# Kernel optimization log

Measured on AMD Instinct MI355X. Metric: run time of the kernel, lower is better.

Reference implementation:

```python
import jax, jax.numpy as jnp
import numpy as np

N_NODES = 100000
N_EDGES = 1600000
F_IN = 256
DIM = 128
N_CLASSES = 16


def gcn_conv(x, W, b, src, dst, num_nodes):
    # PyG GCNConv: add self-loops, symmetric normalization D^-1/2 (A+I) D^-1/2,
    # linear transform then scatter-add aggregation at destination nodes.
    loops = jnp.arange(num_nodes)
    s = jnp.concatenate([src, loops])
    d = jnp.concatenate([dst, loops])
    deg = jax.ops.segment_sum(jnp.ones(d.shape[0], dtype=x.dtype), d, num_segments=num_nodes)
    dinv = jnp.where(deg > 0, jax.lax.rsqrt(deg), jnp.zeros_like(deg))
    norm = dinv[s] * dinv[d]                       # [E+N]
    h = x @ W                                      # [N, out] transform-then-propagate
    msg = h[s] * norm[:, None]                     # gather + scale
    out = jax.ops.segment_sum(msg, d, num_segments=num_nodes)  # scatter-add
    return out + b


def setup_inputs() -> dict:
    key = jax.random.key(0)
    k1, k2, k3, k4 = jax.random.split(key, 4)
    x = jax.random.normal(k1, (N_NODES, F_IN), dtype=jnp.float32)
    edge_index = jax.random.randint(k2, (2, N_EDGES), 0, N_NODES, dtype=jnp.int64)
    W1 = jax.random.normal(k3, (F_IN, DIM), dtype=jnp.float32) * 0.05
    b1 = jnp.zeros((DIM,), dtype=jnp.float32)
    W2 = jax.random.normal(k4, (DIM, N_CLASSES), dtype=jnp.float32) * 0.05
    b2 = jnp.zeros((N_CLASSES,), dtype=jnp.float32)
    return {"x": x, "edge_index": edge_index, "W1": W1, "b1": b1, "W2": W2, "b2": b2}


def reference(x, edge_index, W1, b1, W2, b2):
    # Gcn.forward with num_layers=2 (gcs empty), eval-mode dropout (identity)
    src, dst = edge_index[0], edge_index[1]
    n = x.shape[0]
    h = jax.nn.relu(gcn_conv(x, W1, b1, src, dst, n))
    logits = gcn_conv(h, W2, b2, src, dst, n)
    return jax.nn.log_softmax(logits, axis=-1)
```

## Files before the change

kernel.cpp:

```cpp
#include <hip/hip_runtime.h>
#include <hip/hip_bf16.h>

#define F_IN   256
#define DIM    128
#define NCLS   16
#define BSH    9
#define NBMAX  256
#define CAP    10240
#define PCAP   14336

typedef short bf16x8 __attribute__((ext_vector_type(8)));
typedef float f32x4  __attribute__((ext_vector_type(4)));
typedef float f32x2  __attribute__((ext_vector_type(2)));

__device__ __forceinline__ unsigned short f2bf(float f) {
    union { float f; unsigned u; } v; v.f = f;
    unsigned r = v.u + 0x7fffu + ((v.u >> 16) & 1u);
    return (unsigned short)(r >> 16);
}
__device__ __forceinline__ float bflo(unsigned v) { return __uint_as_float(v << 16); }
__device__ __forceinline__ float bfhi(unsigned v) { return __uint_as_float(v & 0xffff0000u); }


__global__ void binit_kernel(int* __restrict__ bucketCur) {
    int t = threadIdx.x;
    if (t < NBMAX) bucketCur[t] = t * CAP;
}

__global__ __launch_bounds__(1024) void part_kernel(const int* __restrict__ src,
                                                    const int* __restrict__ dst,
                                                    int* __restrict__ bucketCur,
                                                    int2* __restrict__ pairs, int E) {
    __shared__ int hist[NBMAX];
    __shared__ int pos[NBMAX];
    int t = threadIdx.x;
    int base = blockIdx.x * 8192;
    int s[8], d[8];
#pragma unroll
    for (int k = 0; k < 8; k++) {
        int i = base + k * 1024 + t;
        bool v = (i < E);
        s[k] = v ? src[i] : 0;
        d[k] = v ? dst[i] : -1;
    }
    if (t < NBMAX) hist[t] = 0;
    __syncthreads();
#pragma unroll
    for (int k = 0; k < 8; k++)
        if (d[k] >= 0) atomicAdd(&hist[d[k] >> BSH], 1);
    __syncthreads();
    if (t < NBMAX && hist[t]) pos[t] = atomicAdd(&bucketCur[t], hist[t]);
    __syncthreads();
#pragma unroll
    for (int k = 0; k < 8; k++)
        if (d[k] >= 0) {
            int p = atomicAdd(&pos[d[k] >> BSH], 1);
            pairs[p] = make_int2(s[k], d[k]);
        }
}

__global__ __launch_bounds__(256) void csr_kernel(const int2* __restrict__ pairs,
                                                  const int* __restrict__ bucketCur,
                                                  int* __restrict__ rowInfo, float* __restrict__ dinv,
                                                  int* __restrict__ col, int N) {
    __shared__ int cnt[512];
    __shared__ int part[256];
    int b = blockIdx.x, t = threadIdx.x;
    int n0 = b << BSH;
    int nn = N - n0; if (nn > 512) nn = 512;
    int in0 = b * CAP;
    int inEnd = bucketCur[b];
    int out0 = b * PCAP;

    if (t < 256) { cnt[t] = 0; cnt[t + 256] = 0; }
    __syncthreads();
    for (int p = in0 + t; p < inEnd; p += 256)
        atomicAdd(&cnt[pairs[p].y - n0], 1);
    __syncthreads();

    int i0 = t * 2;
    int c0 = cnt[i0], c1 = cnt[i0 + 1];
    int p0 = (c0 + 7) & ~7, p1 = (c1 + 7) & ~7;
    int tsum = p0 + p1;
    part[t] = tsum;
    __syncthreads();
    for (int off = 1; off < 256; off <<= 1) {
        int u = (t >= off) ? part[t - off] : 0;
        __syncthreads();
        part[t] += u;
        __syncthreads();
    }
    int run = out0 + part[t] - tsum;
    int e0 = run, e1 = e0 + p0;
    __syncthreads();
    if (i0 + 0 < nn) { rowInfo[n0 + i0 + 0] = ((e0 >> 3) << 12) | (p0 >> 3); dinv[n0 + i0 + 0] = rsqrtf((float)(c0 + 1)); }
    if (i0 + 1 < nn) { rowInfo[n0 + i0 + 1] = ((e1 >> 3) << 12) | (p1 >> 3); dinv[n0 + i0 + 1] = rsqrtf((float)(c1 + 1)); }
    cnt[i0] = e0; cnt[i0 + 1] = e1;
    __syncthreads();

    for (int p = in0 + t; p < inEnd; p += 256) {
        int2 e = pairs[p];
        int q = atomicAdd(&cnt[e.y - n0], 1);
        col[q] = e.x;
    }
    __syncthreads();
    if (i0 + 0 < nn) for (int q = c0; q < p0; q++) col[e0 + q] = N;
    if (i0 + 1 < nn) for (int q = c1; q < p1; q++) col[e1 + q] = N;
}

__global__ void w1prep_kernel(const float* __restrict__ W1, unsigned short* __restrict__ W1f,
                              unsigned* __restrict__ h1dummy, unsigned* __restrict__ h2dummy) {
    int t = blockIdx.x * blockDim.x + threadIdx.x;
    if (blockIdx.x == 0) {
        if (threadIdx.x < 32) h1dummy[threadIdx.x] = 0;
        else if (threadIdx.x < 40) h2dummy[threadIdx.x - 32] = 0;
    }
    if (t >= 8 * 32 * 16 * 8) return;
    int j = t & 7, c = (t >> 3) & 15, g = (t >> 7) & 31, f = t >> 12;
    W1f[t] = f2bf(W1[(g * 8 + j) * DIM + f * 16 + c]);
}

__global__ __launch_bounds__(256) void gemm1_mfma(const float* __restrict__ X,
                                                  const unsigned short* __restrict__ W1f,
                                                  const float* __restrict__ dinv,
                                                  unsigned char* __restrict__ H1, int M) {
    int tid = threadIdx.x;
    int wm = tid >> 6, l = tid & 63;
    int lr = l & 15, lg = l >> 4;
    int bm = blockIdx.x * 64 + wm * 16;

    f32x4 acc[8];
#pragma unroll
    for (int f = 0; f < 8; f++) acc[f] = (f32x4){0.f, 0.f, 0.f, 0.f};

#pragma unroll
    for (int s = 0; s < 8; s++) {
        int r = bm + lr;
        r = (r < M) ? r : (M - 1);
        const float* xp = X + (size_t)r * F_IN + s * 32 + lg * 8;
        float4 u0 = *(const float4*)xp;
        float4 u1 = *(const float4*)(xp + 4);
        bf16x8 a;
        a[0] = (short)f2bf(u0.x); a[1] = (short)f2bf(u0.y);
        a[2] = (short)f2bf(u0.z); a[3] = (short)f2bf(u0.w);
        a[4] = (short)f2bf(u1.x); a[5] = (short)f2bf(u1.y);
        a[6] = (short)f2bf(u1.z); a[7] = (short)f2bf(u1.w);
#pragma unroll
        for (int f = 0; f < 8; f++) {
            const unsigned short* bp = W1f + ((((f * 32 + s * 4 + lg) * 16) + lr) << 3);
            bf16x8 b = *(const bf16x8*)bp;
            acc[f] = __builtin_amdgcn_mfma_f32_16x16x32_bf16(a, b, acc[f], 0, 0, 0);
        }
    }
#pragma unroll
    for (int r = 0; r < 4; r++) {
        int row = bm + lg * 4 + r;
        if (row < M) {
            float di = dinv[row];
            float v0 = di * acc[0][r], v1 = di * acc[1][r];
            float v2 = di * acc[2][r], v3 = di * acc[3][r];
            float v4 = di * acc[4][r], v5 = di * acc[5][r];
            float v6 = di * acc[6][r], v7 = di * acc[7][r];
            int w0 = __builtin_amdgcn_cvt_pk_fp8_f32(v0, v1, 0, false);
            w0 = __builtin_amdgcn_cvt_pk_fp8_f32(v2, v3, w0, true);
            int w1 = __builtin_amdgcn_cvt_pk_fp8_f32(v4, v5, 0, false);
            w1 = __builtin_amdgcn_cvt_pk_fp8_f32(v6, v7, w1, true);
            uint2 pk; pk.x = (unsigned)w0; pk.y = (unsigned)w1;
            *(uint2*)(H1 + ((size_t)row << 7) + lr * 8) = pk;
        }
    }
}

__global__ __launch_bounds__(256, 8) void agg1_kernel(const unsigned char* __restrict__ H1,
                                                      const int* __restrict__ rowInfo,
                                                      const int* __restrict__ col,
                                                      const float* __restrict__ dinv,
                                                      const float* __restrict__ b1,
                                                      const float* __restrict__ W2,
                                                      unsigned short* __restrict__ H2, int N) {
    __shared__ f32x4 a_lds4[4][32];
    int tid = threadIdx.x;
    int wave = tid >> 6, lane = tid & 63;
    int d = blockIdx.x * 4 + wave;
    int half = lane >> 5;
    int li = lane & 31;
    unsigned kb4 = (unsigned)li * 4;

    float di = 0.f;
    if (d < N) {
        di = dinv[d];
        unsigned sg = *(const unsigned*)(H1 + (((unsigned)d << 7) | kb4));
        if (half) sg = 0u;
        f32x2 acc01 = __builtin_amdgcn_cvt_pk_f32_fp8((int)sg, false);
        f32x2 acc23 = __builtin_amdgcn_cvt_pk_f32_fp8((int)sg, true);

        int info = rowInfo[d];
        int jb = (info >> 12) << 3;
        int jend = jb + ((info & 0xFFF) << 3);
        for (int j0 = jb; j0 < jend; j0 += 64) {
            int cnt = jend - j0; if (cnt > 64) cnt = 64;
            int eidx = col[j0 + lane];
            for (int kk = 0; kk < cnt; kk += 8) {
                int sA = __shfl(eidx, kk + 0 + half);
                int sB = __shfl(eidx, kk + 2 + half);
                int sC = __shfl(eidx, kk + 4 + half);
                int sD = __shfl(eidx, kk + 6 + half);
                unsigned gA = *(const unsigned*)(H1 + (((unsigned)sA << 7) | kb4));
                unsigned gB = *(const unsigned*)(H1 + (((unsigned)sB << 7) | kb4));
                unsigned gC = *(const unsigned*)(H1 + (((unsigned)sC << 7) | kb4));
                unsigned gD = *(const unsigned*)(H1 + (((unsigned)sD << 7) | kb4));
                f32x2 a0 = __builtin_amdgcn_cvt_pk_f32_fp8((int)gA, false);
                f32x2 a1 = __builtin_amdgcn_cvt_pk_f32_fp8((int)gA, true);
                f32x2 b0 = __builtin_amdgcn_cvt_pk_f32_fp8((int)gB, false);
                f32x2 b1v = __builtin_amdgcn_cvt_pk_f32_fp8((int)gB, true);
                f32x2 c0 = __builtin_amdgcn_cvt_pk_f32_fp8((int)gC, false);
                f32x2 c1 = __builtin_amdgcn_cvt_pk_f32_fp8((int)gC, true);
                f32x2 d0 = __builtin_amdgcn_cvt_pk_f32_fp8((int)gD, false);
                f32x2 d1 = __builtin_amdgcn_cvt_pk_f32_fp8((int)gD, true);
                acc01 += (a0 + b0) + (c0 + d0);
                acc23 += (a1 + b1v) + (c1 + d1);
            }
        }
        acc01.x += __shfl_xor(acc01.x, 32);
        acc01.y += __shfl_xor(acc01.y, 32);
        acc23.x += __shfl_xor(acc23.x, 32);
        acc23.y += __shfl_xor(acc23.y, 32);
        if (half == 0) {
            int p0 = li * 4;
            int f0 = ((p0 & 7) << 4) | (p0 >> 3);
            int f1 = (((p0 + 1) & 7) << 4) | ((p0 + 1) >> 3);
            int f2 = (((p0 + 2) & 7) << 4) | ((p0 + 2) >> 3);
            int f3 = (((p0 + 3) & 7) << 4) | ((p0 + 3) >> 3);
            f32x4 a;
            a[0] = fmaxf(fmaf(acc01.x, di, b1[f0]), 0.f);
            a[1] = fmaxf(fmaf(acc01.y, di, b1[f1]), 0.f);
            a[2] = fmaxf(fmaf(acc23.x, di, b1[f2]), 0.f);
            a[3] = fmaxf(fmaf(acc23.y, di, b1[f3]), 0.f);
            a_lds4[wave][li] = a;
        }
    }
    __syncthreads();
    if (d < N) {
        int c = lane & 15, kg = lane >> 4;
        const float* a_ldsf = (const float*)a_lds4[wave];
        const float* w2b = W2 + kg * 64 + c;
        float p = 0.f;
#pragma unroll
        for (int i = 0; i < 32; i++) {
            int w2off = ((i & 7) << 8) + ((i >> 3) << 4);
            p = fmaf(a_ldsf[kg * 32 + i], w2b[w2off], p);
        }
        p += __shfl_xor(p, 16);
        p += __shfl_xor(p, 32);
        if (lane < 16) H2[(size_t)d * NCLS + c] = f2bf(p * di);
    }
}

__global__ __launch_bounds__(256, 8) void agg2_kernel(const unsigned short* __restrict__ H2,
                                                      const int* __restrict__ rowInfo,
                                                      const int* __restrict__ col,
                                                      const float* __restrict__ dinv,
                                                      const float* __restrict__ b2,
                                                      float* __restrict__ OUT, int N) {
    int tid = threadIdx.x;
    int g = tid >> 3, q = tid & 7;
    int d = blockIdx.x * 32 + g;
    if (d >= N) return;
    unsigned cb = (unsigned)q * 4;
    const char* H2b = (const char*)H2;
    float di = dinv[d];
    unsigned u = *(const unsigned*)(H2b + (((unsigned)d << 5) | cb));
    f32x2 acc; acc.x = bflo(u); acc.y = bfhi(u);
    int info = rowInfo[d];
    int jb = (info >> 12) << 3;
    int jend = jb + ((info & 0xFFF) << 3);
    for (int j = jb; j < jend; j += 8) {
        unsigned u0 = *(const unsigned*)(H2b + (((unsigned)col[j + 0] << 5) | cb));
        unsigned u1 = *(const unsigned*)(H2b + (((unsigned)col[j + 1] << 5) | cb));
        unsigned u2 = *(const unsigned*)(H2b + (((unsigned)col[j + 2] << 5) | cb));
        unsigned u3 = *(const unsigned*)(H2b + (((unsigned)col[j + 3] << 5) | cb));
        unsigned u4 = *(const unsigned*)(H2b + (((unsigned)col[j + 4] << 5) | cb));
        unsigned u5 = *(const unsigned*)(H2b + (((unsigned)col[j + 5] << 5) | cb));
        unsigned u6 = *(const unsigned*)(H2b + (((unsigned)col[j + 6] << 5) | cb));
        unsigned u7 = *(const unsigned*)(H2b + (((unsigned)col[j + 7] << 5) | cb));
        f32x2 v0; v0.x = bflo(u0); v0.y = bfhi(u0);
        f32x2 v1; v1.x = bflo(u1); v1.y = bfhi(u1);
        f32x2 v2; v2.x = bflo(u2); v2.y = bfhi(u2);
        f32x2 v3; v3.x = bflo(u3); v3.y = bfhi(u3);
        f32x2 v4; v4.x = bflo(u4); v4.y = bfhi(u4);
        f32x2 v5; v5.x = bflo(u5); v5.y = bfhi(u5);
        f32x2 v6; v6.x = bflo(u6); v6.y = bfhi(u6);
        f32x2 v7; v7.x = bflo(u7); v7.y = bfhi(u7);
        acc += ((v0 + v1) + (v2 + v3)) + ((v4 + v5) + (v6 + v7));
    }
    float l0 = fmaf(acc.x, di, b2[q * 2]);
    float l1 = fmaf(acc.y, di, b2[q * 2 + 1]);
    float m = fmaxf(l0, l1);
    m = fmaxf(m, __shfl_xor(m, 1, 8));
    m = fmaxf(m, __shfl_xor(m, 2, 8));
    m = fmaxf(m, __shfl_xor(m, 4, 8));
    float e = __expf(l0 - m) + __expf(l1 - m);
    e += __shfl_xor(e, 1, 8);
    e += __shfl_xor(e, 2, 8);
    e += __shfl_xor(e, 4, 8);
    float ls = __logf(e);
    float2 o; o.x = l0 - m - ls; o.y = l1 - m - ls;
    *(float2*)(OUT + ((size_t)d << 4) + q * 2) = o;
}

extern "C" void kernel_launch(void* const* d_in, const int* in_sizes, int n_in,
                              void* d_out, int out_size, void* d_ws, size_t ws_size,
                              hipStream_t stream) {
    const float* x  = (const float*)d_in[0];
    const int*   ei = (const int*)d_in[1];
    const float* W1 = (const float*)d_in[2];
    const float* b1 = (const float*)d_in[3];
    const float* W2 = (const float*)d_in[4];
    const float* b2 = (const float*)d_in[5];
    float* out = (float*)d_out;

    const int N = in_sizes[0] / F_IN;
    const int E = in_sizes[1] / 2;
    const int* src = ei;
    const int* dst = ei + E;
    const int nb = (N + (1 << BSH) - 1) >> BSH;

    char* ws = (char*)d_ws;
    size_t off = 0;
    auto alloc = [&](size_t bytes) {
        size_t o = off;
        off += (bytes + 255) & ~(size_t)255;
        return (void*)(ws + o);
    };
    int*            bucketCur   = (int*)alloc(NBMAX * 4);
    int*            rowInfo     = (int*)alloc((size_t)N * 4);
    float*          dinv        = (float*)alloc((size_t)N * 4);
    int*            colw        = (int*)alloc((size_t)NBMAX * PCAP * 4);
    unsigned short* w1f         = (unsigned short*)alloc(32768 * 2);
    unsigned short* h2          = (unsigned short*)alloc((size_t)(N + 1) * NCLS * 2);
    size_t uni = (size_t)NBMAX * CAP * 8;
    size_t h1b = (size_t)(N + 1) * DIM;
    if (h1b > uni) uni = h1b;
    char*           ureg        = (char*)alloc(uni);
    int2*           pairs       = (int2*)ureg;
    unsigned char*  h1          = (unsigned char*)ureg;
    (void)ws_size;

    const int gridE = (E + 8191) / 8192;

    binit_kernel<<<1, NBMAX, 0, stream>>>(bucketCur);
    part_kernel<<<gridE, 1024, 0, stream>>>(src, dst, bucketCur, pairs, E);
    csr_kernel<<<nb, 256, 0, stream>>>(pairs, bucketCur, rowInfo, dinv, colw, N);

    w1prep_kernel<<<128, 256, 0, stream>>>(W1, w1f,
                                           (unsigned*)(h1 + (size_t)N * DIM),
                                           (unsigned*)(h2 + (size_t)N * NCLS));
    gemm1_mfma<<<(N + 63) / 64, 256, 0, stream>>>(x, w1f, dinv, h1, N);
    agg1_kernel<<<(N + 3) / 4, 256, 0, stream>>>(h1, rowInfo, colw, dinv, b1, W2, h2, N);
    agg2_kernel<<<(N + 31) / 32, 256, 0, stream>>>(h2, rowInfo, colw, dinv, b2, out, N);
}
```

Measured before the change: 154.1 us.

## Overlap CSR build with GEMM1 by moving source-side dinv scaling into aggregation

Merges W1 prep with bucket init into one kernel, and fuses CSR construction and the X·W1 MFMA GEMM into a single launch whose blocks split by index. The GEMM no longer needs dinv, so it can run alongside the CSR build. To allow this, the source-side degree normalisation moves into agg1, which gathers dinv per neighbour and uses FMAs. pairs and H1 now get separate buffers instead of sharing one, and row padding grows to multiples of 16 so agg1 can unroll 16 gathers. The costs are more padding entries, extra dinv gathers and shuffles, and fp8 quantisation of unscaled values, which could change accuracy.

New measurement: 143.6 us. 6.8% less time.

```diff
diff --git a/kernel.cpp b/kernel.cpp
--- a/kernel.cpp
+++ b/kernel.cpp
@@ -7,7 +7,7 @@
 #define BSH    9
 #define NBMAX  256
 #define CAP    10240
-#define PCAP   14336
+#define PCAP   18432
 
 typedef short bf16x8 __attribute__((ext_vector_type(8)));
 typedef float f32x4  __attribute__((ext_vector_type(4)));
@@ -21,10 +21,20 @@
 __device__ __forceinline__ float bflo(unsigned v) { return __uint_as_float(v << 16); }
 __device__ __forceinline__ float bfhi(unsigned v) { return __uint_as_float(v & 0xffff0000u); }
 
-
-__global__ void binit_kernel(int* __restrict__ bucketCur) {
-    int t = threadIdx.x;
-    if (t < NBMAX) bucketCur[t] = t * CAP;
+__global__ void init_kernel(const float* __restrict__ W1, unsigned short* __restrict__ W1f,
+                            int* __restrict__ bucketCur,
+                            unsigned* __restrict__ h1dummy, unsigned* __restrict__ h2dummy,
+                            float* __restrict__ dinv, int N) {
+    int t = blockIdx.x * blockDim.x + threadIdx.x;
+    if (blockIdx.x == 0) {
+        bucketCur[threadIdx.x] = threadIdx.x * CAP;
+        if (threadIdx.x < 32) h1dummy[threadIdx.x] = 0;
+        else if (threadIdx.x < 40) h2dummy[threadIdx.x - 32] = 0;
+        else if (threadIdx.x == 40) dinv[N] = 0.f;
+    }
+    if (t >= 8 * 32 * 16 * 8) return;
+    int j = t & 7, c = (t >> 3) & 15, g = (t >> 7) & 31, f = t >> 12;
+    W1f[t] = f2bf(W1[(g * 8 + j) * DIM + f * 16 + c]);
 }
 
 __global__ __launch_bounds__(1024) void part_kernel(const int* __restrict__ src,
@@ -59,114 +69,97 @@
         }
 }
 
-__global__ __launch_bounds__(256) void csr_kernel(const int2* __restrict__ pairs,
-                                                  const int* __restrict__ bucketCur,
-                                                  int* __restrict__ rowInfo, float* __restrict__ dinv,
-                                                  int* __restrict__ col, int N) {
+__global__ __launch_bounds__(256) void csr_gemm_kernel(
+        const int2* __restrict__ pairs, const int* __restrict__ bucketCur,
+        int* __restrict__ rowInfo, float* __restrict__ dinv, int* __restrict__ col,
+        const float* __restrict__ X, const unsigned short* __restrict__ W1f,
+        unsigned char* __restrict__ H1, int N, int nbCsr) {
     __shared__ int cnt[512];
     __shared__ int part[256];
-    int b = blockIdx.x, t = threadIdx.x;
-    int n0 = b << BSH;
-    int nn = N - n0; if (nn > 512) nn = 512;
-    int in0 = b * CAP;
-    int inEnd = bucketCur[b];
-    int out0 = b * PCAP;
-
-    if (t < 256) { cnt[t] = 0; cnt[t + 256] = 0; }
-    __syncthreads();
-    for (int p = in0 + t; p < inEnd; p += 256)
-        atomicAdd(&cnt[pairs[p].y - n0], 1);
-    __syncthreads();
-
-    int i0 = t * 2;
-    int c0 = cnt[i0], c1 = cnt[i0 + 1];
-    int p0 = (c0 + 7) & ~7, p1 = (c1 + 7) & ~7;
-    int tsum = p0 + p1;
-    part[t] = tsum;
-    __syncthreads();
-    for (int off = 1; off < 256; off <<= 1) {
-        int u = (t >= off) ? part[t - off] : 0;
-        __syncthreads();
-        part[t] += u;
-        __syncthreads();
-    }
-    int run = out0 + part[t] - tsum;
-    int e0 = run, e1 = e0 + p0;
-    __syncthreads();
-    if (i0 + 0 < nn) { rowInfo[n0 + i0 + 0] = ((e0 >> 3) << 12) | (p0 >> 3); dinv[n0 + i0 + 0] = rsqrtf((float)(c0 + 1)); }
-    if (i0 + 1 < nn) { rowInfo[n0 + i0 + 1] = ((e1 >> 3) << 12) | (p1 >> 3); dinv[n0 + i0 + 1] = rsqrtf((float)(c1 + 1)); }
-    cnt[i0] = e0; cnt[i0 + 1] = e1;
-    __syncthreads();
-
-    for (int p = in0 + t; p < inEnd; p += 256) {
-        int2 e = pairs[p];
-        int q = atomicAdd(&cnt[e.y - n0], 1);
-        col[q] = e.x;
-    }
-    __syncthreads();
-    if (i0 + 0 < nn) for (int q = c0; q < p0; q++) col[e0 + q] = N;
-    if (i0 + 1 < nn) for (int q = c1; q < p1; q++) col[e1 + q] = N;
-}
-
-__global__ void w1prep_kernel(const float* __restrict__ W1, unsigned short* __restrict__ W1f,
-                              unsigned* __restrict__ h1dummy, unsigned* __restrict__ h2dummy) {
-    int t = blockIdx.x * blockDim.x + threadIdx.x;
-    if (blockIdx.x == 0) {
-        if (threadIdx.x < 32) h1dummy[threadIdx.x] = 0;
-        else if (threadIdx.x < 40) h2dummy[threadIdx.x - 32] = 0;
-    }
-    if (t >= 8 * 32 * 16 * 8) return;
-    int j = t & 7, c = (t >> 3) & 15, g = (t >> 7) & 31, f = t >> 12;
-    W1f[t] = f2bf(W1[(g * 8 + j) * DIM + f * 16 + c]);
-}
-
-__global__ __launch_bounds__(256) void gemm1_mfma(const float* __restrict__ X,
-                                                  const unsigned short* __restrict__ W1f,
-                                                  const float* __restrict__ dinv,
-                                                  unsigned char* __restrict__ H1, int M) {
-    int tid = threadIdx.x;
-    int wm = tid >> 6, l = tid & 63;
-    int lr = l & 15, lg = l >> 4;
-    int bm = blockIdx.x * 64 + wm * 16;
-
-    f32x4 acc[8];
-#pragma unroll
-    for (int f = 0; f < 8; f++) acc[f] = (f32x4){0.f, 0.f, 0.f, 0.f};
-
-#pragma unroll
-    for (int s = 0; s < 8; s++) {
-        int r = bm + lr;
-        r = (r < M) ? r : (M - 1);
-        const float* xp = X + (size_t)r * F_IN + s * 32 + lg * 8;
-        float4 u0 = *(const float4*)xp;
-        float4 u1 = *(const float4*)(xp + 4);
-        bf16x8 a;
-        a[0] = (short)f2bf(u0.x); a[1] = (short)f2bf(u0.y);
-        a[2] = (short)f2bf(u0.z); a[3] = (short)f2bf(u0.w);
-        a[4] = (short)f2bf(u1.x); a[5] = (short)f2bf(u1.y);
-        a[6] = (short)f2bf(u1.z); a[7] = (short)f2bf(u1.w);
-#pragma unroll
-        for (int f = 0; f < 8; f++) {
-            const unsigned short* bp = W1f + ((((f * 32 + s * 4 + lg) * 16) + lr) << 3);
-            bf16x8 b = *(const bf16x8*)bp;
-            acc[f] = __builtin_amdgcn_mfma_f32_16x16x32_bf16(a, b, acc[f], 0, 0, 0);
-        }
-    }
-#pragma unroll
-    for (int r = 0; r < 4; r++) {
-        int row = bm + lg * 4 + r;
-        if (row < M) {
-            float di = dinv[row];
-            float v0 = di * acc[0][r], v1 = di * acc[1][r];
-            float v2 = di * acc[2][r], v3 = di * acc[3][r];
-            float v4 = di * acc[4][r], v5 = di * acc[5][r];
-            float v6 = di * acc[6][r], v7 = di * acc[7][r];
-            int w0 = __builtin_amdgcn_cvt_pk_fp8_f32(v0, v1, 0, false);
-            w0 = __builtin_amdgcn_cvt_pk_fp8_f32(v2, v3, w0, true);
-            int w1 = __builtin_amdgcn_cvt_pk_fp8_f32(v4, v5, 0, false);
-            w1 = __builtin_amdgcn_cvt_pk_fp8_f32(v6, v7, w1, true);
-            uint2 pk; pk.x = (unsigned)w0; pk.y = (unsigned)w1;
-            *(uint2*)(H1 + ((size_t)row << 7) + lr * 8) = pk;
+    int t = threadIdx.x;
+
+    if (blockIdx.x < nbCsr) {
+        int b = blockIdx.x;
+        int n0 = b << BSH;
+        int nn = N - n0; if (nn > 512) nn = 512;
+        int in0 = b * CAP;
+        int inEnd = bucketCur[b];
+        int out0 = b * PCAP;
+
+        cnt[t] = 0; cnt[t + 256] = 0;
+        __syncthreads();
+        for (int p = in0 + t; p < inEnd; p += 256)
+            atomicAdd(&cnt[pairs[p].y - n0], 1);
+        __syncthreads();
+
+        int i0 = t * 2;
+        int c0 = cnt[i0], c1 = cnt[i0 + 1];
+        int p0 = (c0 + 15) & ~15, p1 = (c1 + 15) & ~15;
+        int tsum = p0 + p1;
+        part[t] = tsum;
+        __syncthreads();
+        for (int off = 1; off < 256; off <<= 1) {
+            int u = (t >= off) ? part[t - off] : 0;
+            __syncthreads();
+            part[t] += u;
+            __syncthreads();
+        }
+        int run = out0 + part[t] - tsum;
+        int e0 = run, e1 = e0 + p0;
+        __syncthreads();
+        if (i0 + 0 < nn) { rowInfo[n0 + i0 + 0] = ((e0 >> 4) << 12) | (p0 >> 4); dinv[n0 + i0 + 0] = rsqrtf((float)(c0 + 1)); }
+        if (i0 + 1 < nn) { rowInfo[n0 + i0 + 1] = ((e1 >> 4) << 12) | (p1 >> 4); dinv[n0 + i0 + 1] = rsqrtf((float)(c1 + 1)); }
+        cnt[i0] = e0; cnt[i0 + 1] = e1;
+        __syncthreads();
+
+        for (int p = in0 + t; p < inEnd; p += 256) {
+            int2 e = pairs[p];
+            int q = atomicAdd(&cnt[e.y - n0], 1);
+            col[q] = e.x;
+        }
+        __syncthreads();
+        if (i0 + 0 < nn) for (int q = c0; q < p0; q++) col[e0 + q] = N;
+        if (i0 + 1 < nn) for (int q = c1; q < p1; q++) col[e1 + q] = N;
+    } else {
+        int gb = blockIdx.x - nbCsr;
+        int wm = t >> 6, l = t & 63;
+        int lr = l & 15, lg = l >> 4;
+        int bm = gb * 64 + wm * 16;
+
+        f32x4 acc[8];
+#pragma unroll
+        for (int f = 0; f < 8; f++) acc[f] = (f32x4){0.f, 0.f, 0.f, 0.f};
+
+#pragma unroll
+        for (int s = 0; s < 8; s++) {
+            int r = bm + lr;
+            r = (r < N) ? r : (N - 1);
+            const float* xp = X + (size_t)r * F_IN + s * 32 + lg * 8;
+            float4 u0 = *(const float4*)xp;
+            float4 u1 = *(const float4*)(xp + 4);
+            bf16x8 a;
+            a[0] = (short)f2bf(u0.x); a[1] = (short)f2bf(u0.y);
+            a[2] = (short)f2bf(u0.z); a[3] = (short)f2bf(u0.w);
+            a[4] = (short)f2bf(u1.x); a[5] = (short)f2bf(u1.y);
+            a[6] = (short)f2bf(u1.z); a[7] = (short)f2bf(u1.w);
+#pragma unroll
+            for (int f = 0; f < 8; f++) {
+                const unsigned short* bp = W1f + ((((f * 32 + s * 4 + lg) * 16) + lr) << 3);
+                bf16x8 b = *(const bf16x8*)bp;
+                acc[f] = __builtin_amdgcn_mfma_f32_16x16x32_bf16(a, b, acc[f], 0, 0, 0);
+            }
+        }
+#pragma unroll
+        for (int r = 0; r < 4; r++) {
+            int row = bm + lg * 4 + r;
+            if (row < N) {
+                int w0 = __builtin_amdgcn_cvt_pk_fp8_f32(acc[0][r], acc[1][r], 0, false);
+                w0 = __builtin_amdgcn_cvt_pk_fp8_f32(acc[2][r], acc[3][r], w0, true);
+                int w1 = __builtin_amdgcn_cvt_pk_fp8_f32(acc[4][r], acc[5][r], 0, false);
+                w1 = __builtin_amdgcn_cvt_pk_fp8_f32(acc[6][r], acc[7][r], w1, true);
+                uint2 pk; pk.x = (unsigned)w0; pk.y = (unsigned)w1;
+                *(uint2*)(H1 + ((size_t)row << 7) + lr * 8) = pk;
+            }
         }
     }
 }
@@ -191,34 +184,70 @@
         di = dinv[d];
         unsigned sg = *(const unsigned*)(H1 + (((unsigned)d << 7) | kb4));
         if (half) sg = 0u;
-        f32x2 acc01 = __builtin_amdgcn_cvt_pk_f32_fp8((int)sg, false);
-        f32x2 acc23 = __builtin_amdgcn_cvt_pk_f32_fp8((int)sg, true);
+        f32x2 s0v = __builtin_amdgcn_cvt_pk_f32_fp8((int)sg, false);
+        f32x2 s1v = __builtin_amdgcn_cvt_pk_f32_fp8((int)sg, true);
+        f32x2 acc01, acc23;
+        acc01.x = s0v.x * di; acc01.y = s0v.y * di;
+        acc23.x = s1v.x * di; acc23.y = s1v.y * di;
 
         int info = rowInfo[d];
-        int jb = (info >> 12) << 3;
-        int jend = jb + ((info & 0xFFF) << 3);
+        int jb = (info >> 12) << 4;
+        int jend = jb + ((info & 0xFFF) << 4);
         for (int j0 = jb; j0 < jend; j0 += 64) {
             int cnt = jend - j0; if (cnt > 64) cnt = 64;
             int eidx = col[j0 + lane];
-            for (int kk = 0; kk < cnt; kk += 8) {
-                int sA = __shfl(eidx, kk + 0 + half);
-                int sB = __shfl(eidx, kk + 2 + half);
-                int sC = __shfl(eidx, kk + 4 + half);
-                int sD = __shfl(eidx, kk + 6 + half);
+            if ((unsigned)eidx > (unsigned)N) eidx = N;
+            float dv = dinv[eidx];
+            for (int kk = 0; kk < cnt; kk += 16) {
+                int sA = __shfl(eidx, kk + 0 + half),  sB = __shfl(eidx, kk + 2 + half);
+                int sC = __shfl(eidx, kk + 4 + half),  sD = __shfl(eidx, kk + 6 + half);
+                int sE = __shfl(eidx, kk + 8 + half),  sF = __shfl(eidx, kk + 10 + half);
+                int sG = __shfl(eidx, kk + 12 + half), sH = __shfl(eidx, kk + 14 + half);
+                float vA = __shfl(dv, kk + 0 + half),  vB = __shfl(dv, kk + 2 + half);
+                float vC = __shfl(dv, kk + 4 + half),  vD = __shfl(dv, kk + 6 + half);
+                float vE = __shfl(dv, kk + 8 + half),  vF = __shfl(dv, kk + 10 + half);
+                float vG = __shfl(dv, kk + 12 + half), vH = __shfl(dv, kk + 14 + half);
                 unsigned gA = *(const unsigned*)(H1 + (((unsigned)sA << 7) | kb4));
                 unsigned gB = *(const unsigned*)(H1 + (((unsigned)sB << 7) | kb4));
                 unsigned gC = *(const unsigned*)(H1 + (((unsigned)sC << 7) | kb4));
                 unsigned gD = *(const unsigned*)(H1 + (((unsigned)sD << 7) | kb4));
-                f32x2 a0 = __builtin_amdgcn_cvt_pk_f32_fp8((int)gA, false);
-                f32x2 a1 = __builtin_amdgcn_cvt_pk_f32_fp8((int)gA, true);
-                f32x2 b0 = __builtin_amdgcn_cvt_pk_f32_fp8((int)gB, false);
-                f32x2 b1v = __builtin_amdgcn_cvt_pk_f32_fp8((int)gB, true);
-                f32x2 c0 = __builtin_amdgcn_cvt_pk_f32_fp8((int)gC, false);
-                f32x2 c1 = __builtin_amdgcn_cvt_pk_f32_fp8((int)gC, true);
-                f32x2 d0 = __builtin_amdgcn_cvt_pk_f32_fp8((int)gD, false);
-                f32x2 d1 = __builtin_amdgcn_cvt_pk_f32_fp8((int)gD, true);
-                acc01 += (a0 + b0) + (c0 + d0);
-                acc23 += (a1 + b1v) + (c1 + d1);
+                unsigned gE = *(const unsigned*)(H1 + (((unsigned)sE << 7) | kb4));
+                unsigned gF = *(const unsigned*)(H1 + (((unsigned)sF << 7) | kb4));
+                unsigned gG = *(const unsigned*)(H1 + (((unsigned)sG << 7) | kb4));
+                unsigned gH = *(const unsigned*)(H1 + (((unsigned)sH << 7) | kb4));
+                f32x2 t0, t1;
+                t0 = __builtin_amdgcn_cvt_pk_f32_fp8((int)gA, false);
+                t1 = __builtin_amdgcn_cvt_pk_f32_fp8((int)gA, true);
+                acc01.x = fmaf(t0.x, vA, acc01.x); acc01.y = fmaf(t0.y, vA, acc01.y);
+                acc23.x = fmaf(t1.x, vA, acc23.x); acc23.y = fmaf(t1.y, vA, acc23.y);
+                t0 = __builtin_amdgcn_cvt_pk_f32_fp8((int)gB, false);
+                t1 = __builtin_amdgcn_cvt_pk_f32_fp8((int)gB, true);
+                acc01.x = fmaf(t0.x, vB, acc01.x); acc01.y = fmaf(t0.y, vB, acc01.y);
+                acc23.x = fmaf(t1.x, vB, acc23.x); acc23.y = fmaf(t1.y, vB, acc23.y);
+                t0 = __builtin_amdgcn_cvt_pk_f32_fp8((int)gC, false);
+                t1 = __builtin_amdgcn_cvt_pk_f32_fp8((int)gC, true);
+                acc01.x = fmaf(t0.x, vC, acc01.x); acc01.y = fmaf(t0.y, vC, acc01.y);
+                acc23.x = fmaf(t1.x, vC, acc23.x); acc23.y = fmaf(t1.y, vC, acc23.y);
+                t0 = __builtin_amdgcn_cvt_pk_f32_fp8((int)gD, false);
+                t1 = __builtin_amdgcn_cvt_pk_f32_fp8((int)gD, true);
+                acc01.x = fmaf(t0.x, vD, acc01.x); acc01.y = fmaf(t0.y, vD, acc01.y);
+                acc23.x = fmaf(t1.x, vD, acc23.x); acc23.y = fmaf(t1.y, vD, acc23.y);
+                t0 = __builtin_amdgcn_cvt_pk_f32_fp8((int)gE, false);
+                t1 = __builtin_amdgcn_cvt_pk_f32_fp8((int)gE, true);
+                acc01.x = fmaf(t0.x, vE, acc01.x); acc01.y = fmaf(t0.y, vE, acc01.y);
+                acc23.x = fmaf(t1.x, vE, acc23.x); acc23.y = fmaf(t1.y, vE, acc23.y);
+                t0 = __builtin_amdgcn_cvt_pk_f32_fp8((int)gF, false);
+                t1 = __builtin_amdgcn_cvt_pk_f32_fp8((int)gF, true);
+                acc01.x = fmaf(t0.x, vF, acc01.x); acc01.y = fmaf(t0.y, vF, acc01.y);
+                acc23.x = fmaf(t1.x, vF, acc23.x); acc23.y = fmaf(t1.y, vF, acc23.y);
+                t0 = __builtin_amdgcn_cvt_pk_f32_fp8((int)gG, false);
+                t1 = __builtin_amdgcn_cvt_pk_f32_fp8((int)gG, true);
+                acc01.x = fmaf(t0.x, vG, acc01.x); acc01.y = fmaf(t0.y, vG, acc01.y);
+                acc23.x = fmaf(t1.x, vG, acc23.x); acc23.y = fmaf(t1.y, vG, acc23.y);
+                t0 = __builtin_amdgcn_cvt_pk_f32_fp8((int)gH, false);
+                t1 = __builtin_amdgcn_cvt_pk_f32_fp8((int)gH, true);
+                acc01.x = fmaf(t0.x, vH, acc01.x); acc01.y = fmaf(t0.y, vH, acc01.y);
+                acc23.x = fmaf(t1.x, vH, acc23.x); acc23.y = fmaf(t1.y, vH, acc23.y);
             }
         }
         acc01.x += __shfl_xor(acc01.x, 32);
@@ -272,8 +301,8 @@
     unsigned u = *(const unsigned*)(H2b + (((unsigned)d << 5) | cb));
     f32x2 acc; acc.x = bflo(u); acc.y = bfhi(u);
     int info = rowInfo[d];
-    int jb = (info >> 12) << 3;
-    int jend = jb + ((info & 0xFFF) << 3);
+    int jb = (info >> 12) << 4;
+    int jend = jb + ((info & 0xFFF) << 4);
     for (int j = jb; j < jend; j += 8) {
         unsigned u0 = *(const unsigned*)(H2b + (((unsigned)col[j + 0] << 5) | cb));
         unsigned u1 = *(const unsigned*)(H2b + (((unsigned)col[j + 1] << 5) | cb));
@@ -334,28 +363,23 @@
     };
     int*            bucketCur   = (int*)alloc(NBMAX * 4);
     int*            rowInfo     = (int*)alloc((size_t)N * 4);
-    float*          dinv        = (float*)alloc((size_t)N * 4);
+    float*          dinv        = (float*)alloc((size_t)(N + 1) * 4);
     int*            colw        = (int*)alloc((size_t)NBMAX * PCAP * 4);
     unsigned short* w1f         = (unsigned short*)alloc(32768 * 2);
     unsigned short* h2          = (unsigned short*)alloc((size_t)(N + 1) * NCLS * 2);
-    size_t uni = (size_t)NBMAX * CAP * 8;
-    size_t h1b = (size_t)(N + 1) * DIM;
-    if (h1b > uni) uni = h1b;
-    char*           ureg        = (char*)alloc(uni);
-    int2*           pairs       = (int2*)ureg;
-    unsigned char*  h1          = (unsigned char*)ureg;
+    int2*           pairs       = (int2*)alloc((size_t)NBMAX * CAP * 8);
+    unsigned char*  h1          = (unsigned char*)alloc((size_t)(N + 1) * DIM);
     (void)ws_size;
 
     const int gridE = (E + 8191) / 8192;
 
-    binit_kernel<<<1, NBMAX, 0, stream>>>(bucketCur);
+    init_kernel<<<128, 256, 0, stream>>>(W1, w1f, bucketCur,
+                                         (unsigned*)(h1 + (size_t)N * DIM),
+                                         (unsigned*)(h2 + (size_t)N * NCLS),
+                                         dinv, N);
     part_kernel<<<gridE, 1024, 0, stream>>>(src, dst, bucketCur, pairs, E);
-    csr_kernel<<<nb, 256, 0, stream>>>(pairs, bucketCur, rowInfo, dinv, colw, N);
-
-    w1prep_kernel<<<128, 256, 0, stream>>>(W1, w1f,
-                                           (unsigned*)(h1 + (size_t)N * DIM),
-                                           (unsigned*)(h2 + (size_t)N * NCLS));
-    gemm1_mfma<<<(N + 63) / 64, 256, 0, stream>>>(x, w1f, dinv, h1, N);
+    csr_gemm_kernel<<<nb + (N + 63) / 64, 256, 0, stream>>>(pairs, bucketCur, rowInfo, dinv, colw,
+                                                            x, w1f, h1, N, nb);
     agg1_kernel<<<(N + 3) / 4, 256, 0, stream>>>(h1, rowInfo, colw, dinv, b1, W2, h2, N);
     agg2_kernel<<<(N + 31) / 32, 256, 0, stream>>>(h2, rowInfo, colw, dinv, b2, out, N);
 }
```
